# Kernel tuning notes

Measured on AMD Instinct MI355X. Metric: run time of the kernel, lower is better.

## Reference

```python
import jax, jax.numpy as jnp
import numpy as np

B, S, DIM, H, HD = 2, 2048, 512, 8, 64
VD = DIM // H  # 64
QK = H * HD


def setup_inputs() -> dict:
    key = jax.random.key(0)
    k1, k2, k3, k4, k5 = jax.random.split(key, 5)
    x = jax.random.normal(k1, (B, S, DIM), dtype=jnp.float32)
    mask = jax.random.bernoulli(k2, 0.5, (B, S))
    # per-position rotation matrices, scaled to keep activations O(1)
    rotator = jax.random.normal(k3, (B, S, HD, HD), dtype=jnp.float32) / np.sqrt(HD)
    # torch Linear weights: [out_features, in_features], no bias
    W_trans = jax.random.normal(k4, (2 * QK + DIM, DIM), dtype=jnp.float32) / np.sqrt(DIM)
    W_o = jax.random.normal(k5, (DIM, DIM), dtype=jnp.float32) / np.sqrt(DIM)
    return {"x": x, "mask": mask, "rotator": rotator, "W_trans": W_trans, "W_o": W_o}


def _taylor_attention(qs, ks, vs, mask):
    # 2nd-order Taylor approximation of exp for softmax weights
    # qs/ks: [B,S,H,HD], vs: [B,S,H,VD], mask: [B,S] key mask
    scores = jnp.einsum('bqhd,bkhd->bhqk', qs, ks) / np.sqrt(HD)
    w = 1.0 + scores + 0.5 * scores * scores
    w = jnp.where(mask[:, None, None, :], w, 0.0)
    w = w / jnp.sum(w, axis=-1, keepdims=True)
    out = jnp.einsum('bhqk,bkhd->bqhd', w, vs)
    return out.reshape(out.shape[0], out.shape[1], -1)  # [B,S,DIM]


def reference(x, mask, rotator, W_trans, W_o):
    t = x @ W_trans.T  # [B,S,2*QK+DIM]
    qs = t[..., :QK].reshape(B, S, H, HD)
    ks = t[..., QK:2 * QK].reshape(B, S, H, HD)
    vs = t[..., 2 * QK:].reshape(B, S, H, VD)
    sel = mask[..., None, None]
    qs = jnp.where(sel, jnp.einsum('bsij,bshj->bshi', rotator, qs), qs)
    ks = jnp.where(sel, jnp.einsum('bsij,bshj->bshi', rotator, ks), ks)
    out = _taylor_attention(qs, ks, vs, mask)
    return out @ W_o.T
```

## Files before the change

kernel.cpp:

```cpp
#include <hip/hip_runtime.h>
#include <hip/hip_bf16.h>

#define B_    2
#define S_    2048
#define DIM_  512
#define H_    8
#define HD_   64
#define TOUT_ 1536
#define ROWS_ (B_ * S_)

typedef unsigned short ushort_t;
typedef __attribute__((ext_vector_type(8))) __bf16 bf16x8;
typedef __attribute__((ext_vector_type(4))) float floatx4;

#define AS_GLB __attribute__((address_space(1)))
#define AS_LDS __attribute__((address_space(3)))

__device__ __forceinline__ float bf2f(unsigned int u) { return __uint_as_float(u << 16); }
__device__ __forceinline__ unsigned short f2bfu(float f) {
    unsigned u = __float_as_uint(f);
    unsigned r = (u + 0x7fffu + ((u >> 16) & 1u)) >> 16;
    return (unsigned short)r;
}
__device__ __forceinline__ bf16x8 cvt8(const float* p) {
    float4 a = *reinterpret_cast<const float4*>(p);
    float4 b = *reinterpret_cast<const float4*>(p + 4);
    ushort_t o[8] = {f2bfu(a.x), f2bfu(a.y), f2bfu(a.z), f2bfu(a.w),
                     f2bfu(b.x), f2bfu(b.y), f2bfu(b.z), f2bfu(b.w)};
    return *reinterpret_cast<bf16x8*>(o);
}

__global__ void tmha_detect(const unsigned char* mb, int* flags) {
    __shared__ int s_bf, s_f, s_u8;
    int tid = threadIdx.x;
    if (tid == 0) { s_bf = 0; s_f = 0; s_u8 = 0; }
    __syncthreads();
    int cbf = 0, cf = 0, cu8 = 0;
    for (int i = tid; i < 4096; i += 256) {
        unsigned char v = mb[i];
        if (v == 0x3F || v == 0x80) {
            cf++;
            if ((i & 3) == 1) cbf++;
        } else if (v != 0 && (i & 3) != 0) {
            cu8++;
        }
    }
    atomicAdd(&s_bf, cbf); atomicAdd(&s_f, cf); atomicAdd(&s_u8, cu8);
    __syncthreads();
    if (tid == 0) {
        int mcls;
        if (s_bf > 0)      mcls = 2;
        else if (s_f > 0)  mcls = 3;
        else if (s_u8 > 0) mcls = 0;
        else               mcls = 1;
        flags[1] = mcls;
    }
}

__global__ void tmha_decode_mask(const unsigned char* mb, const int* flags, int* wm) {
    int i = blockIdx.x * 256 + threadIdx.x;
    if (i >= ROWS_) return;
    int cls = flags[1];
    int v;
    if (cls == 0)      v = (mb[i] != 0);
    else if (cls == 1) v = (reinterpret_cast<const int*>(mb)[i] != 0);
    else if (cls == 2) v = ((reinterpret_cast<const unsigned short*>(mb)[i] & 0x7fffu) != 0);
    else               v = ((reinterpret_cast<const unsigned int*>(mb)[i] & 0x7fffffffu) != 0);
    wm[i] = v;
}

__global__ __launch_bounds__(256) void cast_bf16(const float* __restrict__ src,
                                                 ushort_t* __restrict__ dst, int n4) {
    int i = blockIdx.x * 256 + threadIdx.x;
    if (i >= n4) return;
    float4 v = reinterpret_cast<const float4*>(src)[i];
    ushort_t o[4] = {f2bfu(v.x), f2bfu(v.y), f2bfu(v.z), f2bfu(v.w)};
    reinterpret_cast<uint2*>(dst)[i] = *reinterpret_cast<uint2*>(o);
}

template <int TM, int N, int K>
__global__ __launch_bounds__(256) void mfma_gemm_bt(const ushort_t* __restrict__ A,
                                                    const ushort_t* __restrict__ Bm,
                                                    float* __restrict__ C) {
    constexpr int FM = TM / 32;
    __shared__ __align__(16) ushort_t As[TM * 64];
    __shared__ __align__(16) ushort_t Bs[128 * 64];
    int tid = threadIdx.x;
    int lane = tid & 63;
    int wv = tid >> 6;
    int wm = wv >> 1, wn = wv & 1;
    int quad = lane >> 4;
    int mrow = lane & 15;
    int bx = blockIdx.x;
    int by = blockIdx.y;

    floatx4 acc[FM][4];
#pragma unroll
    for (int i = 0; i < FM; i++)
#pragma unroll
        for (int j = 0; j < 4; j++) acc[i][j] = (floatx4){0.f, 0.f, 0.f, 0.f};

    for (int k0 = 0; k0 < K; k0 += 64) {
#pragma unroll
        for (int t = 0; t < TM / 32; t++) {
            int p = (wv * (TM / 32) + t) * 64 + lane;
            int row = p >> 3, cp = p & 7;
            int gc = cp ^ (row & 7);
            const ushort_t* ga = A + (size_t)(by * TM + row) * K + k0 + gc * 8;
            __builtin_amdgcn_global_load_lds((const AS_GLB unsigned int*)ga,
                                             (AS_LDS unsigned int*)&As[(size_t)(wv * (TM / 32) + t) * 64 * 8],
                                             16, 0, 0);
        }
#pragma unroll
        for (int t = 0; t < 4; t++) {
            int p = (wv * 4 + t) * 64 + lane;
            int row = p >> 3, cp = p & 7;
            int gc = cp ^ (row & 7);
            const ushort_t* gb = Bm + (size_t)(bx * 128 + row) * K + k0 + gc * 8;
            __builtin_amdgcn_global_load_lds((const AS_GLB unsigned int*)gb,
                                             (AS_LDS unsigned int*)&Bs[(size_t)(wv * 4 + t) * 64 * 8],
                                             16, 0, 0);
        }
        __syncthreads();
#pragma unroll
        for (int ks = 0; ks < 64; ks += 32) {
            int c = (ks >> 3) + quad;
            bf16x8 af[FM], bf[4];
#pragma unroll
            for (int i = 0; i < FM; i++) {
                int row = wm * (TM / 2) + i * 16 + mrow;
                int pos = row * 8 + (c ^ (row & 7));
                af[i] = *reinterpret_cast<const bf16x8*>(&As[pos * 8]);
            }
#pragma unroll
            for (int j = 0; j < 4; j++) {
                int row = wn * 64 + j * 16 + mrow;
                int pos = row * 8 + (c ^ (row & 7));
                bf[j] = *reinterpret_cast<const bf16x8*>(&Bs[pos * 8]);
            }
#pragma unroll
            for (int i = 0; i < FM; i++)
#pragma unroll
                for (int j = 0; j < 4; j++)
                    acc[i][j] = __builtin_amdgcn_mfma_f32_16x16x32_bf16(af[i], bf[j], acc[i][j], 0, 0, 0);
        }
        __syncthreads();
    }

    int col0 = bx * 128 + wn * 64 + mrow;
    int row0 = by * TM + wm * (TM / 2) + quad * 4;
#pragma unroll
    for (int i = 0; i < FM; i++)
#pragma unroll
        for (int j = 0; j < 4; j++)
#pragma unroll
            for (int r = 0; r < 4; r++)
                C[(size_t)(row0 + i * 16 + r) * N + col0 + j * 16] = acc[i][j][r];
}

__global__ __launch_bounds__(256) void rot_qk_mfma(const float* __restrict__ t,
                                                   const float* __restrict__ rotG,
                                                   const int* __restrict__ wm,
                                                   ushort_t* __restrict__ Qb,
                                                   ushort_t* __restrict__ Kb) {
    int lane = threadIdx.x & 63;
    int wv = threadIdx.x >> 6;
    int row = blockIdx.x * 4 + wv;
    int b = row >> 11, s = row & 2047;
    int lm = lane & 15, quad = lane >> 4;
    const float* trow = t + (size_t)row * TOUT_;

    if (wm[row]) {
        bf16x8 af[2];
#pragma unroll
        for (int kc = 0; kc < 2; kc++)
            af[kc] = cvt8(trow + lm * 64 + kc * 32 + quad * 8);

        const float* R = rotG + (size_t)row * 4096;
        floatx4 dacc[4];
#pragma unroll
        for (int nb = 0; nb < 4; nb++) dacc[nb] = (floatx4){0.f, 0.f, 0.f, 0.f};
#pragma unroll
        for (int nb = 0; nb < 4; nb++)
#pragma unroll
            for (int kc = 0; kc < 2; kc++) {
                bf16x8 bfr = cvt8(R + (size_t)(nb * 16 + lm) * 64 + kc * 32 + quad * 8);
                dacc[nb] = __builtin_amdgcn_mfma_f32_16x16x32_bf16(af[kc], bfr, dacc[nb], 0, 0, 0);
            }
#pragma unroll
        for (int nb = 0; nb < 4; nb++)
#pragma unroll
            for (int r = 0; r < 4; r++) {
                int vec = quad * 4 + r;
                int h = vec & 7;
                ushort_t* dst = (vec >= 8 ? Kb : Qb);
                dst[((size_t)(b * 8 + h) * 2048 + s) * 64 + nb * 16 + lm] = f2bfu(dacc[nb][r]);
            }
    } else {
#pragma unroll
        for (int nb = 0; nb < 4; nb++)
#pragma unroll
            for (int r = 0; r < 4; r++) {
                int vec = quad * 4 + r;
                int h = vec & 7;
                float v = trow[vec * 64 + nb * 16 + lm];
                ushort_t* dst = (vec >= 8 ? Kb : Qb);
                dst[((size_t)(b * 8 + h) * 2048 + s) * 64 + nb * 16 + lm] = f2bfu(v);
            }
    }
}

__global__ __launch_bounds__(256) void prep_vt(const float* __restrict__ t,
                                               const int* __restrict__ wm,
                                               ushort_t* __restrict__ VtG) {
    __shared__ float tile[64][65];
    __shared__ float mrow[64];
    int st = blockIdx.x;
    int bh = blockIdx.y;
    int b = bh >> 3, h = bh & 7;
    int tid = threadIdx.x;
    if (tid < 64) mrow[tid] = wm[b * 2048 + st * 64 + tid] ? 1.0f : 0.0f;
#pragma unroll
    for (int i = 0; i < 4; i++) {
        int q = i * 256 + tid;
        int r = q >> 4, c4 = (q & 15) * 4;
        float4 v = *reinterpret_cast<const float4*>(
            t + (size_t)(b * 2048 + st * 64 + r) * TOUT_ + 1024 + h * 64 + c4);
        tile[r][c4] = v.x; tile[r][c4 + 1] = v.y; tile[r][c4 + 2] = v.z; tile[r][c4 + 3] = v.w;
    }
    __syncthreads();
#pragma unroll
    for (int i = 0; i < 8; i++) {
        int e = i * 256 + tid;
        int d = e >> 5, sl = (e & 31) * 2;
        float v0 = tile[sl][d] * mrow[sl];
        float v1 = tile[sl + 1][d] * mrow[sl + 1];
        unsigned int u = (unsigned)f2bfu(v0) | ((unsigned)f2bfu(v1) << 16);
        *reinterpret_cast<unsigned int*>(VtG + ((size_t)bh * 65 + d) * 2048 + st * 64 + sl) = u;
    }
    if (tid < 32) {
        int sl = tid * 2;
        unsigned m0 = mrow[sl]     != 0.f ? 0x3F80u : 0u;
        unsigned m1 = mrow[sl + 1] != 0.f ? 0x3F80u : 0u;
        *reinterpret_cast<unsigned int*>(VtG + ((size_t)bh * 65 + 64) * 2048 + st * 64 + sl) = m0 | (m1 << 16);
    }
}

__global__ __launch_bounds__(128) void tmha_attn_mfma(const ushort_t* __restrict__ Qb,
                                                      const ushort_t* __restrict__ Kb,
                                                      const ushort_t* __restrict__ VtG,
                                                      ushort_t* __restrict__ attnAb) {
    __shared__ __align__(16) ushort_t Ks[1024 * 8];
    __shared__ __align__(16) ushort_t Vs[1280 * 8];
    __shared__ __align__(16) ushort_t Ps[1024 * 8];
    int tid = threadIdx.x;
    int lane = tid & 63;
    int wv = tid >> 6;
    int lm = lane & 15;
    int quad = lane >> 4;
    int qt = blockIdx.x;
    int h = blockIdx.y;
    int b = blockIdx.z;
    int bh = b * 8 + h;

    for (int i = tid; i < 960; i += 128)
        reinterpret_cast<unsigned int*>(&Vs[1040 * 8])[i] = 0u;

    bf16x8 qf[2][2];
#pragma unroll
    for (int mi = 0; mi < 2; mi++) {
        const ushort_t* qp = Qb + ((size_t)bh * 2048 + qt * 64 + wv * 32 + mi * 16 + lm) * 64 + quad * 8;
        qf[mi][0] = *reinterpret_cast<const bf16x8*>(qp);
        qf[mi][1] = *reinterpret_cast<const bf16x8*>(qp + 32);
    }

    floatx4 oacc[2][5];
#pragma unroll
    for (int mi = 0; mi < 2; mi++)
#pragma unroll
        for (int j = 0; j < 5; j++) oacc[mi][j] = (floatx4){0.f, 0.f, 0.f, 0.f};

    for (int kt = 0; kt < S_; kt += 128) {
#pragma unroll
        for (int t4 = 0; t4 < 8; t4++) {
            int p = (wv * 8 + t4) * 64 + lane;
            int row = p >> 3, cp = p & 7;
            int gc = cp ^ (row & 7);
            const ushort_t* g = Kb + ((size_t)bh * 2048 + kt + row) * 64 + gc * 8;
            __builtin_amdgcn_global_load_lds((const AS_GLB unsigned int*)g,
                                             (AS_LDS unsigned int*)&Ks[(size_t)(wv * 8 + t4) * 64 * 8],
                                             16, 0, 0);
        }
#pragma unroll
        for (int t4 = 0; t4 < 8; t4++) {
            int p = (wv * 8 + t4) * 64 + lane;
            int row = p >> 4, cp = p & 15;
            int gc = cp ^ (row & 15);
            const ushort_t* g = VtG + ((size_t)bh * 65 + row) * 2048 + kt + gc * 8;
            __builtin_amdgcn_global_load_lds((const AS_GLB unsigned int*)g,
                                             (AS_LDS unsigned int*)&Vs[(size_t)(wv * 8 + t4) * 64 * 8],
                                             16, 0, 0);
        }
        if (tid < 64) {
            unsigned int mv = *reinterpret_cast<const unsigned int*>(
                VtG + ((size_t)bh * 65 + 64) * 2048 + kt + tid * 2);
            reinterpret_cast<unsigned int*>(&Vs[1024 * 8])[tid] = mv;
        }
        __syncthreads();

        floatx4 sacc[2][8];
#pragma unroll
        for (int mi = 0; mi < 2; mi++)
#pragma unroll
            for (int j = 0; j < 8; j++) sacc[mi][j] = (floatx4){0.f, 0.f, 0.f, 0.f};
#pragma unroll
        for (int j = 0; j < 8; j++) {
            int row = j * 16 + lm;
#pragma unroll
            for (int kc = 0; kc < 2; kc++) {
                int c = kc * 4 + quad;
                int pos = row * 8 + (c ^ (row & 7));
                bf16x8 bk = *reinterpret_cast<const bf16x8*>(&Ks[pos * 8]);
                sacc[0][j] = __builtin_amdgcn_mfma_f32_16x16x32_bf16(qf[0][kc], bk, sacc[0][j], 0, 0, 0);
                sacc[1][j] = __builtin_amdgcn_mfma_f32_16x16x32_bf16(qf[1][kc], bk, sacc[1][j], 0, 0, 0);
            }
        }

#pragma unroll
        for (int mi = 0; mi < 2; mi++)
#pragma unroll
            for (int j = 0; j < 8; j++)
#pragma unroll
                for (int r = 0; r < 4; r++) {
                    float s = sacc[mi][j][r];
                    float wgt = fmaf(s, fmaf(s, 0.0078125f, 0.125f), 1.0f);
                    int m = wv * 32 + mi * 16 + quad * 4 + r;
                    int col = j * 16 + lm;
                    int cw = col >> 3;
                    int pos = m * 16 + (cw ^ (m & 15));
                    Ps[pos * 8 + (col & 7)] = f2bfu(wgt);
                }
        __syncthreads();

#pragma unroll
        for (int kc = 0; kc < 4; kc++) {
            int c = kc * 4 + quad;
            bf16x8 pa[2];
#pragma unroll
            for (int mi = 0; mi < 2; mi++) {
                int row = wv * 32 + mi * 16 + lm;
                int pos = row * 16 + (c ^ (row & 15));
                pa[mi] = *reinterpret_cast<const bf16x8*>(&Ps[pos * 8]);
            }
#pragma unroll
            for (int j = 0; j < 5; j++) {
                int vrow = j * 16 + lm;
                int vpos = vrow * 16 + (c ^ (vrow & 15));
                bf16x8 vb = *reinterpret_cast<const bf16x8*>(&Vs[vpos * 8]);
                oacc[0][j] = __builtin_amdgcn_mfma_f32_16x16x32_bf16(pa[0], vb, oacc[0][j], 0, 0, 0);
                oacc[1][j] = __builtin_amdgcn_mfma_f32_16x16x32_bf16(pa[1], vb, oacc[1][j], 0, 0, 0);
            }
        }
        __syncthreads();
    }

#pragma unroll
    for (int mi = 0; mi < 2; mi++) {
        float den[4];
#pragma unroll
        for (int r = 0; r < 4; r++) den[r] = __shfl(oacc[mi][4][r], quad * 16, 64);
#pragma unroll
        for (int j = 0; j < 4; j++) {
            int col = h * 64 + j * 16 + lm;
#pragma unroll
            for (int r = 0; r < 4; r++) {
                float v = oacc[mi][j][r] / den[r];
                attnAb[(size_t)(b * 2048 + qt * 64 + wv * 32 + mi * 16 + quad * 4 + r) * DIM_ + col] = f2bfu(v);
            }
        }
    }
}

extern "C" void kernel_launch(void* const* d_in, const int* in_sizes, int n_in,
                              void* d_out, int out_size, void* d_ws, size_t ws_size,
                              hipStream_t stream) {
    (void)in_sizes; (void)n_in; (void)out_size; (void)ws_size;
    const float* x    = (const float*)d_in[0];
    const void*  mask = d_in[1];
    const float* rot  = (const float*)d_in[2];
    const float* Wt   = (const float*)d_in[3];
    const float* Wo   = (const float*)d_in[4];

    char* ws = (char*)d_ws;
    int* flags       = (int*)ws;
    int* wmask       = (int*)(ws + 64);
    float* t         = (float*)(ws + 32768);
    ushort_t* Xb     = (ushort_t*)(ws + 25198592);
    ushort_t* Wtb    = (ushort_t*)(ws + 29392896);
    ushort_t* Wob    = (ushort_t*)(ws + 30965760);
    ushort_t* Qb     = (ushort_t*)(ws + 31490048);
    ushort_t* Kb     = (ushort_t*)(ws + 35684352);
    ushort_t* VtG    = (ushort_t*)(ws + 39878656);
    ushort_t* attnAb = (ushort_t*)(ws + 44138496);

    tmha_detect<<<1, 256, 0, stream>>>((const unsigned char*)mask, flags);
    tmha_decode_mask<<<16, 256, 0, stream>>>((const unsigned char*)mask, flags, wmask);

    cast_bf16<<<(ROWS_ * DIM_ / 4 + 255) / 256, 256, 0, stream>>>(x, Xb, ROWS_ * DIM_ / 4);
    cast_bf16<<<(TOUT_ * DIM_ / 4 + 255) / 256, 256, 0, stream>>>(Wt, Wtb, TOUT_ * DIM_ / 4);
    cast_bf16<<<(DIM_ * DIM_ / 4 + 255) / 256, 256, 0, stream>>>(Wo, Wob, DIM_ * DIM_ / 4);

    {
        dim3 grid(TOUT_ / 128, ROWS_ / 64);
        mfma_gemm_bt<64, TOUT_, DIM_><<<grid, 256, 0, stream>>>(Xb, Wtb, t);
    }

    rot_qk_mfma<<<ROWS_ / 4, 256, 0, stream>>>(t, rot, wmask, Qb, Kb);

    {
        dim3 grid(32, 16);
        prep_vt<<<grid, 256, 0, stream>>>(t, wmask, VtG);
    }

    {
        dim3 grid(32, 8, 2);
        tmha_attn_mfma<<<grid, 128, 0, stream>>>(Qb, Kb, VtG, attnAb);
    }

    {
        dim3 grid(DIM_ / 128, ROWS_ / 64);
        mfma_gemm_bt<64, DIM_, DIM_><<<grid, 256, 0, stream>>>(attnAb, Wob, (float*)d_out);
    }
}
```

Measured before the change: 204.2 us.

## Split attention over key halves with four waves per block and a combine kernel

The attention kernel now splits the key sequence into two halves across grid z and uses four waves per block, each handling 16 query rows instead of 32. This quadruples the number of waves in flight so the GPU is better occupied. Unnormalized fp32 numerators and denominators are written to workspace that reuses the t buffer, and a new combine kernel sums the halves, normalizes and converts to bf16. The cost is extra global traffic for the partial results and one more launch.

Result: no change. 200.3 us (-2.0%).

```diff
diff --git a/kernel.cpp b/kernel.cpp
--- a/kernel.cpp
+++ b/kernel.cpp
@@ -246,10 +246,11 @@
     }
 }
 
-__global__ __launch_bounds__(128) void tmha_attn_mfma(const ushort_t* __restrict__ Qb,
+__global__ __launch_bounds__(256) void tmha_attn_mfma(const ushort_t* __restrict__ Qb,
                                                       const ushort_t* __restrict__ Kb,
                                                       const ushort_t* __restrict__ VtG,
-                                                      ushort_t* __restrict__ attnAb) {
+                                                      float* __restrict__ numer,
+                                                      float* __restrict__ den) {
     __shared__ __align__(16) ushort_t Ks[1024 * 8];
     __shared__ __align__(16) ushort_t Vs[1280 * 8];
     __shared__ __align__(16) ushort_t Ps[1024 * 8];
@@ -260,45 +261,44 @@
     int quad = lane >> 4;
     int qt = blockIdx.x;
     int h = blockIdx.y;
-    int b = blockIdx.z;
+    int z = blockIdx.z;
+    int b = z >> 1;
+    int ks = z & 1;
     int bh = b * 8 + h;
 
-    for (int i = tid; i < 960; i += 128)
+    for (int i = tid; i < 960; i += 256)
         reinterpret_cast<unsigned int*>(&Vs[1040 * 8])[i] = 0u;
 
-    bf16x8 qf[2][2];
-#pragma unroll
-    for (int mi = 0; mi < 2; mi++) {
-        const ushort_t* qp = Qb + ((size_t)bh * 2048 + qt * 64 + wv * 32 + mi * 16 + lm) * 64 + quad * 8;
-        qf[mi][0] = *reinterpret_cast<const bf16x8*>(qp);
-        qf[mi][1] = *reinterpret_cast<const bf16x8*>(qp + 32);
-    }
-
-    floatx4 oacc[2][5];
-#pragma unroll
-    for (int mi = 0; mi < 2; mi++)
-#pragma unroll
-        for (int j = 0; j < 5; j++) oacc[mi][j] = (floatx4){0.f, 0.f, 0.f, 0.f};
-
-    for (int kt = 0; kt < S_; kt += 128) {
-#pragma unroll
-        for (int t4 = 0; t4 < 8; t4++) {
-            int p = (wv * 8 + t4) * 64 + lane;
+    bf16x8 qf[2];
+    {
+        const ushort_t* qp = Qb + ((size_t)bh * 2048 + qt * 64 + wv * 16 + lm) * 64 + quad * 8;
+        qf[0] = *reinterpret_cast<const bf16x8*>(qp);
+        qf[1] = *reinterpret_cast<const bf16x8*>(qp + 32);
+    }
+
+    floatx4 oacc[5];
+#pragma unroll
+    for (int j = 0; j < 5; j++) oacc[j] = (floatx4){0.f, 0.f, 0.f, 0.f};
+
+    for (int kt = ks * 1024; kt < ks * 1024 + 1024; kt += 128) {
+#pragma unroll
+        for (int t4 = 0; t4 < 4; t4++) {
+            int p = (wv * 4 + t4) * 64 + lane;
             int row = p >> 3, cp = p & 7;
             int gc = cp ^ (row & 7);
             const ushort_t* g = Kb + ((size_t)bh * 2048 + kt + row) * 64 + gc * 8;
             __builtin_amdgcn_global_load_lds((const AS_GLB unsigned int*)g,
-                                             (AS_LDS unsigned int*)&Ks[(size_t)(wv * 8 + t4) * 64 * 8],
+                                             (AS_LDS unsigned int*)&Ks[(size_t)(wv * 4 + t4) * 64 * 8],
                                              16, 0, 0);
         }
 #pragma unroll
-        for (int t4 = 0; t4 < 8; t4++) {
-            int p = (wv * 8 + t4) * 64 + lane;
+        for (int t4 = 0; t4 < 4; t4++) {
+            int p = (wv * 4 + t4) * 64 + lane;
             int row = p >> 4, cp = p & 15;
             int gc = cp ^ (row & 15);
             const ushort_t* g = VtG + ((size_t)bh * 65 + row) * 2048 + kt + gc * 8;
             __builtin_amdgcn_global_load_lds((const AS_GLB unsigned int*)g,
-                                             (AS_LDS unsigned int*)&Vs[(size_t)(wv * 8 + t4) * 64 * 8],
+                                             (AS_LDS unsigned int*)&Vs[(size_t)(wv * 4 + t4) * 64 * 8],
                                              16, 0, 0);
         }
         if (tid < 64) {
@@ -308,11 +308,9 @@
         }
         __syncthreads();
 
-        floatx4 sacc[2][8];
-#pragma unroll
-        for (int mi = 0; mi < 2; mi++)
-#pragma unroll
-            for (int j = 0; j < 8; j++) sacc[mi][j] = (floatx4){0.f, 0.f, 0.f, 0.f};
+        floatx4 sacc[8];
+#pragma unroll
+        for (int j = 0; j < 8; j++) sacc[j] = (floatx4){0.f, 0.f, 0.f, 0.f};
 #pragma unroll
         for (int j = 0; j < 8; j++) {
             int row = j * 16 + lm;
@@ -321,64 +319,70 @@
                 int c = kc * 4 + quad;
                 int pos = row * 8 + (c ^ (row & 7));
                 bf16x8 bk = *reinterpret_cast<const bf16x8*>(&Ks[pos * 8]);
-                sacc[0][j] = __builtin_amdgcn_mfma_f32_16x16x32_bf16(qf[0][kc], bk, sacc[0][j], 0, 0, 0);
-                sacc[1][j] = __builtin_amdgcn_mfma_f32_16x16x32_bf16(qf[1][kc], bk, sacc[1][j], 0, 0, 0);
-            }
-        }
-
-#pragma unroll
-        for (int mi = 0; mi < 2; mi++)
-#pragma unroll
-            for (int j = 0; j < 8; j++)
-#pragma unroll
-                for (int r = 0; r < 4; r++) {
-                    float s = sacc[mi][j][r];
-                    float wgt = fmaf(s, fmaf(s, 0.0078125f, 0.125f), 1.0f);
-                    int m = wv * 32 + mi * 16 + quad * 4 + r;
-                    int col = j * 16 + lm;
-                    int cw = col >> 3;
-                    int pos = m * 16 + (cw ^ (m & 15));
-                    Ps[pos * 8 + (col & 7)] = f2bfu(wgt);
-                }
+                sacc[j] = __builtin_amdgcn_mfma_f32_16x16x32_bf16(qf[kc], bk, sacc[j], 0, 0, 0);
+            }
+        }
+
+#pragma unroll
+        for (int j = 0; j < 8; j++)
+#pragma unroll
+            for (int r = 0; r < 4; r++) {
+                float s = sacc[j][r];
+                float wgt = fmaf(s, fmaf(s, 0.0078125f, 0.125f), 1.0f);
+                int m = wv * 16 + quad * 4 + r;
+                int col = j * 16 + lm;
+                int cw = col >> 3;
+                int pos = m * 16 + (cw ^ (m & 15));
+                Ps[pos * 8 + (col & 7)] = f2bfu(wgt);
+            }
         __syncthreads();
 
 #pragma unroll
-        for (int kc = 0; kc < 4; kc++) {
-            int c = kc * 4 + quad;
-            bf16x8 pa[2];
-#pragma unroll
-            for (int mi = 0; mi < 2; mi++) {
-                int row = wv * 32 + mi * 16 + lm;
-                int pos = row * 16 + (c ^ (row & 15));
-                pa[mi] = *reinterpret_cast<const bf16x8*>(&Ps[pos * 8]);
-            }
-#pragma unroll
-            for (int j = 0; j < 5; j++) {
-                int vrow = j * 16 + lm;
+        for (int j = 0; j < 5; j++) {
+            int vrow = j * 16 + lm;
+#pragma unroll
+            for (int kc = 0; kc < 4; kc++) {
+                int c = kc * 4 + quad;
+                int ppos = (wv * 16 + lm) * 16 + (c ^ lm);
+                bf16x8 pa = *reinterpret_cast<const bf16x8*>(&Ps[ppos * 8]);
                 int vpos = vrow * 16 + (c ^ (vrow & 15));
                 bf16x8 vb = *reinterpret_cast<const bf16x8*>(&Vs[vpos * 8]);
-                oacc[0][j] = __builtin_amdgcn_mfma_f32_16x16x32_bf16(pa[0], vb, oacc[0][j], 0, 0, 0);
-                oacc[1][j] = __builtin_amdgcn_mfma_f32_16x16x32_bf16(pa[1], vb, oacc[1][j], 0, 0, 0);
+                oacc[j] = __builtin_amdgcn_mfma_f32_16x16x32_bf16(pa, vb, oacc[j], 0, 0, 0);
             }
         }
         __syncthreads();
     }
 
 #pragma unroll
-    for (int mi = 0; mi < 2; mi++) {
-        float den[4];
-#pragma unroll
-        for (int r = 0; r < 4; r++) den[r] = __shfl(oacc[mi][4][r], quad * 16, 64);
-#pragma unroll
-        for (int j = 0; j < 4; j++) {
-            int col = h * 64 + j * 16 + lm;
-#pragma unroll
-            for (int r = 0; r < 4; r++) {
-                float v = oacc[mi][j][r] / den[r];
-                attnAb[(size_t)(b * 2048 + qt * 64 + wv * 32 + mi * 16 + quad * 4 + r) * DIM_ + col] = f2bfu(v);
-            }
-        }
-    }
+    for (int j = 0; j < 4; j++)
+#pragma unroll
+        for (int r = 0; r < 4; r++) {
+            int qrow = b * 2048 + qt * 64 + wv * 16 + quad * 4 + r;
+            numer[((size_t)ks * ROWS_ + qrow) * DIM_ + h * 64 + j * 16 + lm] = oacc[j][r];
+        }
+    if (lm == 0) {
+#pragma unroll
+        for (int r = 0; r < 4; r++) {
+            int qrow = b * 2048 + qt * 64 + wv * 16 + quad * 4 + r;
+            den[((size_t)ks * ROWS_ + qrow) * 8 + h] = oacc[4][r];
+        }
+    }
+}
+
+__global__ __launch_bounds__(256) void attn_combine(const float* __restrict__ numer,
+                                                    const float* __restrict__ den,
+                                                    ushort_t* __restrict__ attnAb) {
+    int i = blockIdx.x * 256 + threadIdx.x;
+    int row = i >> 7;
+    int c4 = (i & 127) * 4;
+    int h = c4 >> 6;
+    float4 n0 = *reinterpret_cast<const float4*>(&numer[(size_t)row * DIM_ + c4]);
+    float4 n1 = *reinterpret_cast<const float4*>(&numer[((size_t)ROWS_ + row) * DIM_ + c4]);
+    float d = den[(size_t)row * 8 + h] + den[((size_t)ROWS_ + row) * 8 + h];
+    float inv = 1.0f / d;
+    ushort_t o[4] = {f2bfu((n0.x + n1.x) * inv), f2bfu((n0.y + n1.y) * inv),
+                     f2bfu((n0.z + n1.z) * inv), f2bfu((n0.w + n1.w) * inv)};
+    *reinterpret_cast<uint2*>(&attnAb[(size_t)row * DIM_ + c4]) = *reinterpret_cast<uint2*>(o);
 }
 
 extern "C" void kernel_launch(void* const* d_in, const int* in_sizes, int n_in,
@@ -402,6 +406,8 @@
     ushort_t* Kb     = (ushort_t*)(ws + 35684352);
     ushort_t* VtG    = (ushort_t*)(ws + 39878656);
     ushort_t* attnAb = (ushort_t*)(ws + 44138496);
+    float* numer     = t;
+    float* den       = (float*)(ws + 32768 + 16777216);
 
     tmha_detect<<<1, 256, 0, stream>>>((const unsigned char*)mask, flags);
     tmha_decode_mask<<<16, 256, 0, stream>>>((const unsigned char*)mask, flags, wmask);
@@ -423,9 +429,10 @@
     }
 
     {
-        dim3 grid(32, 8, 2);
-        tmha_attn_mfma<<<grid, 128, 0, stream>>>(Qb, Kb, VtG, attnAb);
-    }
+        dim3 grid(32, 8, 4);
+        tmha_attn_mfma<<<grid, 256, 0, stream>>>(Qb, Kb, VtG, numer, den);
+    }
+    attn_combine<<<(ROWS_ * 128) / 256, 256, 0, stream>>>(numer, den, attnAb);
 
     {
         dim3 grid(DIM_ / 128, ROWS_ / 64);
```
